# Performance work log

Measured on AMD Instinct MI355X. Metric: run time of the kernel, lower is better.

## Reference

```python
import jax, jax.numpy as jnp
import numpy as np

N_LAYERS = 3


def setup_inputs() -> dict:
    key = jax.random.key(0)
    ks = jax.random.split(key, 7)
    n_users, n_items, d = 200000, 100000, 64
    n_nodes = n_users + n_items
    n_edges = 2000000
    return {
        "user_embeddings_weight": jax.random.normal(ks[0], (n_users, d), dtype=jnp.float32) * 0.1,
        "item_embeddings_weight": jax.random.normal(ks[1], (n_items, d), dtype=jnp.float32) * 0.1,
        "adj_vals": jax.random.uniform(ks[2], (n_edges,), dtype=jnp.float32),
        "adj_rows": jax.random.randint(ks[3], (n_edges,), 0, n_nodes, dtype=jnp.int32),
        "adj_cols": jax.random.randint(ks[4], (n_edges,), 0, n_nodes, dtype=jnp.int32),
        "user_indices": jax.random.randint(ks[5], (16384,), 0, n_users, dtype=jnp.int32),
        "item_indices": jax.random.randint(ks[6], (16384,), 0, n_items, dtype=jnp.int32),
    }


def reference(user_embeddings_weight, item_embeddings_weight, adj_vals, adj_rows, adj_cols, user_indices, item_indices):
    n_users = user_embeddings_weight.shape[0]
    n_nodes = n_users + item_embeddings_weight.shape[0]
    # layer-0 embeddings: concat users then items -> (N, d)
    emb = jnp.concatenate([user_embeddings_weight, item_embeddings_weight], axis=0)
    acc = emb  # running sum over layers (fuses stack+mean)
    cur = emb
    for _ in range(N_LAYERS):
        # SpMM in COO form: out[r] += val * cur[c]
        cur = jax.ops.segment_sum(adj_vals[:, None] * cur[adj_cols], adj_rows, num_segments=n_nodes)
        acc = acc + cur
    final = acc / jnp.float32(N_LAYERS + 1)  # mean over (n_layers+1) layer outputs
    user_emb = final[:n_users][user_indices]
    item_emb = final[n_users:][item_indices]
    return (user_emb, item_emb)
```

## Files before the change

### kernel.cpp

```cpp
#include <hip/hip_runtime.h>

#define D 64
#define RB 512
#define RB_SHIFT 9
#define COL_BITS 19
#define COL_MASK ((1u << COL_BITS) - 1u)
#define CAP 4096
#define NBMAX 640
#define TILE 4096

__device__ __forceinline__ float bf_lo(unsigned u) { return __uint_as_float(u << 16); }
__device__ __forceinline__ float bf_hi(unsigned u) { return __uint_as_float(u & 0xffff0000u); }
__device__ __forceinline__ unsigned pack_bf2(float a, float b) {
    unsigned ua = __float_as_uint(a), ub = __float_as_uint(b);
    ua += 0x7fffu + ((ua >> 16) & 1u);
    ub += 0x7fffu + ((ub >> 16) & 1u);
    return (ua >> 16) | (ub & 0xffff0000u);
}


__global__ __launch_bounds__(256) void k_tobf(
    const float* __restrict__ src, unsigned* __restrict__ dst, int n2)
{
    int stride = gridDim.x * 256;
    for (int i = blockIdx.x * 256 + threadIdx.x; i < n2; i += stride) {
        float2 v = ((const float2*)src)[i];
        dst[i] = pack_bf2(v.x, v.y);
    }
}

__global__ __launch_bounds__(256) void k_gather_init(
    const float* __restrict__ uw, const float* __restrict__ iw,
    const int* __restrict__ ui, const int* __restrict__ ii,
    float* __restrict__ out, int nq)
{
    int t = blockIdx.x * 256 + threadIdx.x;
    int total = nq * D;
    if (t < total) {
        int q = t >> 6, d = t & 63;
        out[t] = uw[ui[q] * D + d];
    } else if (t < 2 * total) {
        int u = t - total;
        int q = u >> 6, d = u & 63;
        out[t] = iw[ii[q] * D + d];
    }
}

__global__ __launch_bounds__(256) void k_gather_acc_bf(
    const uint2* __restrict__ src,
    const int* __restrict__ ui, const int* __restrict__ ii,
    int n_users, float* __restrict__ out, int nq, float scale)
{
    int lane16 = threadIdx.x & 15;
    int q = blockIdx.x * 16 + (threadIdx.x >> 4);
    if (q >= 2 * nq) return;
    int node = (q < nq) ? ui[q] : n_users + ii[q - nq];
    uint2 x = src[(size_t)node * 16 + lane16];
    float4* o = (float4*)&out[(size_t)q * D + lane16 * 4];
    float4 v = *o;
    v.x = (v.x + bf_lo(x.x)) * scale;
    v.y = (v.y + bf_hi(x.x)) * scale;
    v.z = (v.z + bf_lo(x.y)) * scale;
    v.w = (v.w + bf_hi(x.y)) * scale;
    *o = v;
}


__global__ __launch_bounds__(256) void k_bcount(
    const int* __restrict__ rows, int* __restrict__ bcnt, int ne, int nb)
{
    __shared__ int sh[NBMAX];
    int tid = threadIdx.x;
    int base = blockIdx.x * TILE;
    int end = base + TILE; if (end > ne) end = ne;
    for (int b = tid; b < nb; b += 256) sh[b] = 0;
    __syncthreads();
    for (int e = base + tid; e < end; e += 256)
        atomicAdd(&sh[rows[e] >> RB_SHIFT], 1);
    __syncthreads();
    for (int b = tid; b < nb; b += 256)
        if (sh[b]) atomicAdd(&bcnt[b], sh[b]);
}

__global__ __launch_bounds__(1024) void k_bscan(
    const int* __restrict__ bcnt, int* __restrict__ bstart,
    int* __restrict__ bktFill, int nb)
{
    __shared__ int s[1024];
    int t = threadIdx.x;
    int v = (t < nb) ? bcnt[t] : 0;
    s[t] = v; __syncthreads();
    for (int off = 1; off < 1024; off <<= 1) {
        int x = (t >= off) ? s[t - off] : 0;
        __syncthreads();
        s[t] += x;
        __syncthreads();
    }
    int excl = s[t] - v;
    if (t <= nb) {
        bstart[t] = excl;
        if (t < nb) bktFill[t] = excl;
    }
}

__global__ __launch_bounds__(256) void k_binpart(
    const float* __restrict__ vals, const int* __restrict__ rows,
    const int* __restrict__ cols,
    int* __restrict__ bucketFill, int2* __restrict__ staging,
    int ne, int nb)
{
    __shared__ int shist[NBMAX];
    __shared__ int sgb[NBMAX];
    int tid = threadIdx.x;
    int base = blockIdx.x * TILE;

    for (int b = tid; b < nb; b += 256) shist[b] = 0;
    __syncthreads();

    int myb[TILE / 256];
    int myr[TILE / 256];
    for (int k = 0; k < TILE / 256; ++k) {
        int e = base + k * 256 + tid;
        int b = -1, r = 0;
        if (e < ne) {
            r = rows[e];
            b = r >> RB_SHIFT;
            atomicAdd(&shist[b], 1);
        }
        myb[k] = b; myr[k] = r;
    }
    __syncthreads();
    for (int b = tid; b < nb; b += 256) {
        int c = shist[b];
        sgb[b] = (c > 0) ? atomicAdd(&bucketFill[b], c) : 0;
        shist[b] = 0;
    }
    __syncthreads();
    for (int k = 0; k < TILE / 256; ++k) {
        int e = base + k * 256 + tid;
        if (e >= ne) continue;
        int b = myb[k];
        int lofs = atomicAdd(&shist[b], 1);
        int2 pk;
        pk.x = (int)((((unsigned)myr[k] & (RB - 1)) << COL_BITS) | (unsigned)cols[e]);
        pk.y = __float_as_int(vals[e]);
        staging[sgb[b] + lofs] = pk;
    }
}

__global__ __launch_bounds__(256) void k_place3(
    const int* __restrict__ bstart, const int2* __restrict__ staging,
    int* __restrict__ rstart, int* __restrict__ cnt,
    int2* __restrict__ cedge, int n_nodes, int ne)
{
    __shared__ int hist[RB];
    __shared__ int excl[RB];
    __shared__ int ss[256];
    __shared__ int2 ebuf[CAP];
    int tid = threadIdx.x;
    int b = blockIdx.x;
    int rowbase = b << RB_SHIFT;
    int s = bstart[b], e = bstart[b + 1];
    int m = e - s;

    for (int i = tid; i < RB; i += 256) hist[i] = 0;
    __syncthreads();
    for (int p = s + tid; p < e; p += 256)
        atomicAdd(&hist[((unsigned)staging[p].x) >> COL_BITS], 1);
    __syncthreads();

    int c0 = hist[2 * tid], c1 = hist[2 * tid + 1];
    int sum = c0 + c1;
    ss[tid] = sum; __syncthreads();
    for (int off = 1; off < 256; off <<= 1) {
        int x = (tid >= off) ? ss[tid - off] : 0;
        __syncthreads();
        ss[tid] += x;
        __syncthreads();
    }
    int ex = ss[tid] - sum;
    excl[2 * tid] = ex;
    excl[2 * tid + 1] = ex + c0;
    __syncthreads();

    for (int i = tid; i < RB; i += 256) {
        int r = rowbase + i;
        if (r < n_nodes) { rstart[r] = s + excl[i]; cnt[r] = hist[i]; }
    }
    __syncthreads();
    for (int i = tid; i < RB; i += 256) hist[i] = excl[i];
    __syncthreads();

    if (m <= CAP) {
        for (int p = s + tid; p < e; p += 256) {
            int2 pk = staging[p];
            int lr = ((unsigned)pk.x) >> COL_BITS;
            int pos = atomicAdd(&hist[lr], 1);
            pk.x = (int)((unsigned)pk.x & COL_MASK);
            ebuf[pos] = pk;
        }
        __syncthreads();
        for (int p = tid; p < m; p += 256)
            cedge[s + p] = ebuf[p];
    } else {
        for (int p = s + tid; p < e; p += 256) {
            int2 pk = staging[p];
            int lr = ((unsigned)pk.x) >> COL_BITS;
            int pos = atomicAdd(&hist[lr], 1);
            pk.x = (int)((unsigned)pk.x & COL_MASK);
            cedge[s + pos] = pk;
        }
    }
}

__global__ __launch_bounds__(256) void k_mark(
    const int* __restrict__ rstart, const int* __restrict__ cnt,
    const int2* __restrict__ cedge,
    const int* __restrict__ ui, const int* __restrict__ ii,
    int n_users, unsigned char* __restrict__ flag, int nq)
{
    int q = blockIdx.x * 256 + threadIdx.x;
    if (q >= 2 * nq) return;
    int node = (q < nq) ? ui[q] : n_users + ii[q - nq];
    flag[node] = 1;
    int s = rstart[node], dg = cnt[node];
    for (int j = 0; j < dg; ++j) flag[cedge[s + j].x] = 1;
}

__global__ __launch_bounds__(256) void k_spmm_bf(
    const int* __restrict__ rstart, const int* __restrict__ cnt,
    const int2* __restrict__ cedge,
    const uint2* __restrict__ src,
    uint2* __restrict__ dst, int n_nodes,
    const unsigned char* __restrict__ flag)
{
    int lane16 = threadIdx.x & 15;
    int row = blockIdx.x * 16 + (threadIdx.x >> 4);
    if (row >= n_nodes) return;
    if (flag && !flag[row]) return;

    int s = rstart[row], dg = cnt[row];
    float a0 = 0, a1 = 0, a2 = 0, a3 = 0;
    int j = 0;
    for (; j + 3 < dg; j += 4) {
        int2 e0 = cedge[s + j],     e1 = cedge[s + j + 1];
        int2 e2 = cedge[s + j + 2], e3 = cedge[s + j + 3];
        uint2 x0 = src[(size_t)e0.x * 16 + lane16];
        uint2 x1 = src[(size_t)e1.x * 16 + lane16];
        uint2 x2 = src[(size_t)e2.x * 16 + lane16];
        uint2 x3 = src[(size_t)e3.x * 16 + lane16];
        float v0 = __int_as_float(e0.y), v1 = __int_as_float(e1.y);
        float v2 = __int_as_float(e2.y), v3 = __int_as_float(e3.y);
        a0 += v0 * bf_lo(x0.x); a1 += v0 * bf_hi(x0.x); a2 += v0 * bf_lo(x0.y); a3 += v0 * bf_hi(x0.y);
        a0 += v1 * bf_lo(x1.x); a1 += v1 * bf_hi(x1.x); a2 += v1 * bf_lo(x1.y); a3 += v1 * bf_hi(x1.y);
        a0 += v2 * bf_lo(x2.x); a1 += v2 * bf_hi(x2.x); a2 += v2 * bf_lo(x2.y); a3 += v2 * bf_hi(x2.y);
        a0 += v3 * bf_lo(x3.x); a1 += v3 * bf_hi(x3.x); a2 += v3 * bf_lo(x3.y); a3 += v3 * bf_hi(x3.y);
    }
    for (; j < dg; ++j) {
        int2 e0 = cedge[s + j];
        uint2 x0 = src[(size_t)e0.x * 16 + lane16];
        float v0 = __int_as_float(e0.y);
        a0 += v0 * bf_lo(x0.x); a1 += v0 * bf_hi(x0.x); a2 += v0 * bf_lo(x0.y); a3 += v0 * bf_hi(x0.y);
    }
    uint2 o;
    o.x = pack_bf2(a0, a1);
    o.y = pack_bf2(a2, a3);
    dst[(size_t)row * 16 + lane16] = o;
}

__global__ __launch_bounds__(256) void k_final_bf(
    const int* __restrict__ rstart, const int* __restrict__ cnt,
    const int2* __restrict__ cedge,
    const uint2* __restrict__ src,
    const int* __restrict__ ui, const int* __restrict__ ii,
    int n_users, float* __restrict__ out, int nq, float scale)
{
    int lane16 = threadIdx.x & 15;
    int q = blockIdx.x * 16 + (threadIdx.x >> 4);
    if (q >= 2 * nq) return;
    int node = (q < nq) ? ui[q] : n_users + ii[q - nq];

    int s = rstart[node], dg = cnt[node];
    float4* op = (float4*)&out[(size_t)q * D + lane16 * 4];
    float4 a = *op;
    int j = 0;
    for (; j + 1 < dg; j += 2) {
        int2 e0 = cedge[s + j], e1 = cedge[s + j + 1];
        uint2 x0 = src[(size_t)e0.x * 16 + lane16];
        uint2 x1 = src[(size_t)e1.x * 16 + lane16];
        float v0 = __int_as_float(e0.y), v1 = __int_as_float(e1.y);
        a.x += v0 * bf_lo(x0.x) + v1 * bf_lo(x1.x);
        a.y += v0 * bf_hi(x0.x) + v1 * bf_hi(x1.x);
        a.z += v0 * bf_lo(x0.y) + v1 * bf_lo(x1.y);
        a.w += v0 * bf_hi(x0.y) + v1 * bf_hi(x1.y);
    }
    if (j < dg) {
        int2 e0 = cedge[s + j];
        uint2 x0 = src[(size_t)e0.x * 16 + lane16];
        float v0 = __int_as_float(e0.y);
        a.x += v0 * bf_lo(x0.x); a.y += v0 * bf_hi(x0.x);
        a.z += v0 * bf_lo(x0.y); a.w += v0 * bf_hi(x0.y);
    }
    a.x *= scale; a.y *= scale; a.z *= scale; a.w *= scale;
    *op = a;
}


__global__ __launch_bounds__(256) void k_gather_acc(
    const float* __restrict__ src,
    const int* __restrict__ ui, const int* __restrict__ ii,
    int n_users, float* __restrict__ out, int nq, float scale)
{
    int t = blockIdx.x * 256 + threadIdx.x;
    int total = nq * D;
    if (t < total) {
        int q = t >> 6, d = t & 63;
        out[t] = (out[t] + src[ui[q] * D + d]) * scale;
    } else if (t < 2 * total) {
        int u = t - total;
        int q = u >> 6, d = u & 63;
        out[t] = (out[t] + src[(n_users + ii[q]) * D + d]) * scale;
    }
}

__global__ __launch_bounds__(256) void k_spmm_l0(
    const float* __restrict__ vals, const int* __restrict__ rows,
    const int* __restrict__ cols,
    const float* __restrict__ uw, const float* __restrict__ iw, int n_users,
    float* __restrict__ dst, int n_edges)
{
    int total = n_edges * D;
    int stride = gridDim.x * 256;
    for (int t = blockIdx.x * 256 + threadIdx.x; t < total; t += stride) {
        int e = t >> 6, d = t & 63;
        float v = vals[e];
        int c = cols[e], r = rows[e];
        float x = (c < n_users) ? uw[c * D + d] : iw[(c - n_users) * D + d];
        atomicAdd(dst + r * D + d, v * x);
    }
}

__global__ __launch_bounds__(256) void k_spmm(
    const float* __restrict__ vals, const int* __restrict__ rows,
    const int* __restrict__ cols,
    const float* __restrict__ src, float* __restrict__ dst, int n_edges)
{
    int total = n_edges * D;
    int stride = gridDim.x * 256;
    for (int t = blockIdx.x * 256 + threadIdx.x; t < total; t += stride) {
        int e = t >> 6, d = t & 63;
        float v = vals[e];
        int c = cols[e], r = rows[e];
        atomicAdd(dst + r * D + d, v * src[c * D + d]);
    }
}


extern "C" void kernel_launch(void* const* d_in, const int* in_sizes, int n_in,
                              void* d_out, int out_size, void* d_ws, size_t ws_size,
                              hipStream_t stream) {
    const float* uw   = (const float*)d_in[0];
    const float* iw   = (const float*)d_in[1];
    const float* vals = (const float*)d_in[2];
    const int*   rows = (const int*)d_in[3];
    const int*   cols = (const int*)d_in[4];
    const int*   ui   = (const int*)d_in[5];
    const int*   ii   = (const int*)d_in[6];
    float* out = (float*)d_out;

    const int n_users = in_sizes[0] / D;
    const int n_items = in_sizes[1] / D;
    const int n_nodes = n_users + n_items;
    const int n_edges = in_sizes[2];
    const int nq      = in_sizes[5];

    const int nb = (n_nodes + RB - 1) / RB;

    size_t off = 0;
    int* cnt     = (int*)((char*)d_ws + off); off += (size_t)n_nodes * 4;
    int* rstart  = (int*)((char*)d_ws + off); off += (size_t)n_nodes * 4;
    int* bstart  = (int*)((char*)d_ws + off); off += 4096 * 4;
    int* bcnt    = (int*)((char*)d_ws + off); off += 4096 * 4;
    int* bktFill = (int*)((char*)d_ws + off); off += 4096 * 4;
    unsigned char* flag = (unsigned char*)((char*)d_ws + off);
    off += ((size_t)n_nodes + 255) & ~(size_t)255;
    size_t big = off;

    size_t coff = big;
    unsigned* embB  = (unsigned*)((char*)d_ws + coff); coff += (size_t)n_nodes * D * 2;
    unsigned* bufAh = (unsigned*)((char*)d_ws + coff); coff += (size_t)n_nodes * D * 2;
    unsigned* bufBh = (unsigned*)((char*)d_ws + coff); coff += (size_t)n_nodes * D * 2;
    int2* cedge   = (int2*)((char*)d_ws + coff); coff += (size_t)n_edges * 8;
    int2* staging = (int2*)((char*)d_ws + coff); coff += (size_t)n_edges * 8;

    size_t foff = big;
    float* bufA = (float*)((char*)d_ws + foff); foff += (size_t)n_nodes * D * 4;
    float* bufB = (float*)((char*)d_ws + foff); foff += (size_t)n_nodes * D * 4;

    const int gq = (2 * nq * D + 255) / 256;
    const bool csr_ok = (coff <= ws_size) && (nb < 1024) &&
                        (nb + 1 <= NBMAX) && (n_nodes < (1 << COL_BITS));

    if (csr_ok) {
        k_tobf<<<2048, 256, 0, stream>>>(uw, embB, n_users * (D / 2));
        k_tobf<<<2048, 256, 0, stream>>>(iw, embB + (size_t)n_users * (D / 2),
                                         n_items * (D / 2));

        hipMemsetAsync(bcnt, 0, 4096 * 4, stream);
        hipMemsetAsync(flag, 0, (size_t)n_nodes, stream);
        k_bcount<<<(n_edges + TILE - 1) / TILE, 256, 0, stream>>>(rows, bcnt, n_edges, nb);
        k_bscan<<<1, 1024, 0, stream>>>(bcnt, bstart, bktFill, nb);
        k_binpart<<<(n_edges + TILE - 1) / TILE, 256, 0, stream>>>(
            vals, rows, cols, bktFill, staging, n_edges, nb);
        k_place3<<<nb, 256, 0, stream>>>(bstart, staging, rstart, cnt,
                                         cedge, n_nodes, n_edges);
        k_mark<<<(2 * nq + 255) / 256, 256, 0, stream>>>(
            rstart, cnt, cedge, ui, ii, n_users, flag, nq);

        k_gather_init<<<gq, 256, 0, stream>>>(uw, iw, ui, ii, out, nq);

        const int gs = (n_nodes + 15) / 16;
        const int gq16 = (2 * nq + 15) / 16;
        k_spmm_bf<<<gs, 256, 0, stream>>>(rstart, cnt, cedge, (const uint2*)embB,
                                          (uint2*)bufAh, n_nodes, nullptr);
        k_gather_acc_bf<<<gq16, 256, 0, stream>>>((const uint2*)bufAh, ui, ii,
                                                  n_users, out, nq, 1.0f);
        k_spmm_bf<<<gs, 256, 0, stream>>>(rstart, cnt, cedge, (const uint2*)bufAh,
                                          (uint2*)bufBh, n_nodes, flag);
        k_gather_acc_bf<<<gq16, 256, 0, stream>>>((const uint2*)bufBh, ui, ii,
                                                  n_users, out, nq, 1.0f);
        k_final_bf<<<gq16, 256, 0, stream>>>(rstart, cnt, cedge, (const uint2*)bufBh,
                                             ui, ii, n_users, out, nq, 0.25f);
    } else {
        hipMemsetAsync(bufA, 0, 2 * (size_t)n_nodes * D * 4, stream);
        const int gs = 8192;
        k_gather_init<<<gq, 256, 0, stream>>>(uw, iw, ui, ii, out, nq);
        k_spmm_l0<<<gs, 256, 0, stream>>>(vals, rows, cols, uw, iw, n_users, bufA, n_edges);
        k_gather_acc<<<gq, 256, 0, stream>>>(bufA, ui, ii, n_users, out, nq, 1.0f);
        k_spmm<<<gs, 256, 0, stream>>>(vals, rows, cols, bufA, bufB, n_edges);
        k_gather_acc<<<gq, 256, 0, stream>>>(bufB, ui, ii, n_users, out, nq, 1.0f);
        hipMemsetAsync(bufA, 0, (size_t)n_nodes * D * 4, stream);
        k_spmm<<<gs, 256, 0, stream>>>(vals, rows, cols, bufB, bufA, n_edges);
        k_gather_acc<<<gq, 256, 0, stream>>>(bufA, ui, ii, n_users, out, nq, 0.25f);
    }
}
```

Baseline: 354.6 us.

## Fuse gather/accumulate into final kernel, widen SpMM loads to 16 bytes

```diff
diff --git a/kernel.cpp b/kernel.cpp
--- a/kernel.cpp
+++ b/kernel.cpp
@@ -19,50 +19,17 @@
 }
 
 
-__global__ __launch_bounds__(256) void k_tobf(
-    const float* __restrict__ src, unsigned* __restrict__ dst, int n2)
+__global__ __launch_bounds__(256) void k_tobf2(
+    const float* __restrict__ uw, const float* __restrict__ iw,
+    unsigned* __restrict__ dst, int n2u, int n2i)
 {
     int stride = gridDim.x * 256;
-    for (int i = blockIdx.x * 256 + threadIdx.x; i < n2; i += stride) {
-        float2 v = ((const float2*)src)[i];
+    int total = n2u + n2i;
+    for (int i = blockIdx.x * 256 + threadIdx.x; i < total; i += stride) {
+        float2 v = (i < n2u) ? ((const float2*)uw)[i]
+                             : ((const float2*)iw)[i - n2u];
         dst[i] = pack_bf2(v.x, v.y);
     }
-}
-
-__global__ __launch_bounds__(256) void k_gather_init(
-    const float* __restrict__ uw, const float* __restrict__ iw,
-    const int* __restrict__ ui, const int* __restrict__ ii,
-    float* __restrict__ out, int nq)
-{
-    int t = blockIdx.x * 256 + threadIdx.x;
-    int total = nq * D;
-    if (t < total) {
-        int q = t >> 6, d = t & 63;
-        out[t] = uw[ui[q] * D + d];
-    } else if (t < 2 * total) {
-        int u = t - total;
-        int q = u >> 6, d = u & 63;
-        out[t] = iw[ii[q] * D + d];
-    }
-}
-
-__global__ __launch_bounds__(256) void k_gather_acc_bf(
-    const uint2* __restrict__ src,
-    const int* __restrict__ ui, const int* __restrict__ ii,
-    int n_users, float* __restrict__ out, int nq, float scale)
-{
-    int lane16 = threadIdx.x & 15;
-    int q = blockIdx.x * 16 + (threadIdx.x >> 4);
-    if (q >= 2 * nq) return;
-    int node = (q < nq) ? ui[q] : n_users + ii[q - nq];
-    uint2 x = src[(size_t)node * 16 + lane16];
-    float4* o = (float4*)&out[(size_t)q * D + lane16 * 4];
-    float4 v = *o;
-    v.x = (v.x + bf_lo(x.x)) * scale;
-    v.y = (v.y + bf_hi(x.x)) * scale;
-    v.z = (v.z + bf_lo(x.y)) * scale;
-    v.w = (v.w + bf_hi(x.y)) * scale;
-    *o = v;
 }
 
 
@@ -227,84 +194,130 @@
     for (int j = 0; j < dg; ++j) flag[cedge[s + j].x] = 1;
 }
 
-__global__ __launch_bounds__(256) void k_spmm_bf(
+__global__ __launch_bounds__(256) void k_spmm_bf8(
     const int* __restrict__ rstart, const int* __restrict__ cnt,
     const int2* __restrict__ cedge,
-    const uint2* __restrict__ src,
-    uint2* __restrict__ dst, int n_nodes,
+    const uint4* __restrict__ src,
+    uint4* __restrict__ dst, int n_nodes,
     const unsigned char* __restrict__ flag)
 {
-    int lane16 = threadIdx.x & 15;
-    int row = blockIdx.x * 16 + (threadIdx.x >> 4);
+    int lane8 = threadIdx.x & 7;
+    int row = blockIdx.x * 32 + (threadIdx.x >> 3);
     if (row >= n_nodes) return;
     if (flag && !flag[row]) return;
 
     int s = rstart[row], dg = cnt[row];
-    float a0 = 0, a1 = 0, a2 = 0, a3 = 0;
+    float a0 = 0, a1 = 0, a2 = 0, a3 = 0, a4 = 0, a5 = 0, a6 = 0, a7 = 0;
     int j = 0;
     for (; j + 3 < dg; j += 4) {
         int2 e0 = cedge[s + j],     e1 = cedge[s + j + 1];
         int2 e2 = cedge[s + j + 2], e3 = cedge[s + j + 3];
-        uint2 x0 = src[(size_t)e0.x * 16 + lane16];
-        uint2 x1 = src[(size_t)e1.x * 16 + lane16];
-        uint2 x2 = src[(size_t)e2.x * 16 + lane16];
-        uint2 x3 = src[(size_t)e3.x * 16 + lane16];
+        uint4 x0 = src[(size_t)e0.x * 8 + lane8];
+        uint4 x1 = src[(size_t)e1.x * 8 + lane8];
+        uint4 x2 = src[(size_t)e2.x * 8 + lane8];
+        uint4 x3 = src[(size_t)e3.x * 8 + lane8];
         float v0 = __int_as_float(e0.y), v1 = __int_as_float(e1.y);
         float v2 = __int_as_float(e2.y), v3 = __int_as_float(e3.y);
         a0 += v0 * bf_lo(x0.x); a1 += v0 * bf_hi(x0.x); a2 += v0 * bf_lo(x0.y); a3 += v0 * bf_hi(x0.y);
+        a4 += v0 * bf_lo(x0.z); a5 += v0 * bf_hi(x0.z); a6 += v0 * bf_lo(x0.w); a7 += v0 * bf_hi(x0.w);
         a0 += v1 * bf_lo(x1.x); a1 += v1 * bf_hi(x1.x); a2 += v1 * bf_lo(x1.y); a3 += v1 * bf_hi(x1.y);
+        a4 += v1 * bf_lo(x1.z); a5 += v1 * bf_hi(x1.z); a6 += v1 * bf_lo(x1.w); a7 += v1 * bf_hi(x1.w);
         a0 += v2 * bf_lo(x2.x); a1 += v2 * bf_hi(x2.x); a2 += v2 * bf_lo(x2.y); a3 += v2 * bf_hi(x2.y);
+        a4 += v2 * bf_lo(x2.z); a5 += v2 * bf_hi(x2.z); a6 += v2 * bf_lo(x2.w); a7 += v2 * bf_hi(x2.w);
         a0 += v3 * bf_lo(x3.x); a1 += v3 * bf_hi(x3.x); a2 += v3 * bf_lo(x3.y); a3 += v3 * bf_hi(x3.y);
+        a4 += v3 * bf_lo(x3.z); a5 += v3 * bf_hi(x3.z); a6 += v3 * bf_lo(x3.w); a7 += v3 * bf_hi(x3.w);
     }
     for (; j < dg; ++j) {
         int2 e0 = cedge[s + j];
-        uint2 x0 = src[(size_t)e0.x * 16 + lane16];
+        uint4 x0 = src[(size_t)e0.x * 8 + lane8];
         float v0 = __int_as_float(e0.y);
         a0 += v0 * bf_lo(x0.x); a1 += v0 * bf_hi(x0.x); a2 += v0 * bf_lo(x0.y); a3 += v0 * bf_hi(x0.y);
-    }
-    uint2 o;
+        a4 += v0 * bf_lo(x0.z); a5 += v0 * bf_hi(x0.z); a6 += v0 * bf_lo(x0.w); a7 += v0 * bf_hi(x0.w);
+    }
+    uint4 o;
     o.x = pack_bf2(a0, a1);
     o.y = pack_bf2(a2, a3);
-    dst[(size_t)row * 16 + lane16] = o;
-}
-
-__global__ __launch_bounds__(256) void k_final_bf(
+    o.z = pack_bf2(a4, a5);
+    o.w = pack_bf2(a6, a7);
+    dst[(size_t)row * 8 + lane8] = o;
+}
+
+__global__ __launch_bounds__(256) void k_final_all(
     const int* __restrict__ rstart, const int* __restrict__ cnt,
     const int2* __restrict__ cedge,
-    const uint2* __restrict__ src,
+    const float* __restrict__ uw, const float* __restrict__ iw,
+    const uint4* __restrict__ bufA, const uint4* __restrict__ bufB,
     const int* __restrict__ ui, const int* __restrict__ ii,
     int n_users, float* __restrict__ out, int nq, float scale)
 {
-    int lane16 = threadIdx.x & 15;
-    int q = blockIdx.x * 16 + (threadIdx.x >> 4);
+    int lane8 = threadIdx.x & 7;
+    int q = blockIdx.x * 32 + (threadIdx.x >> 3);
     if (q >= 2 * nq) return;
     int node = (q < nq) ? ui[q] : n_users + ii[q - nq];
 
+    const float* embrow = (node < n_users) ? &uw[(size_t)node * D]
+                                           : &iw[(size_t)(node - n_users) * D];
+    float4 e0 = ((const float4*)embrow)[lane8 * 2];
+    float4 e1 = ((const float4*)embrow)[lane8 * 2 + 1];
+    uint4 xa = bufA[(size_t)node * 8 + lane8];
+    uint4 xb = bufB[(size_t)node * 8 + lane8];
+    float a0 = e0.x + bf_lo(xa.x) + bf_lo(xb.x);
+    float a1 = e0.y + bf_hi(xa.x) + bf_hi(xb.x);
+    float a2 = e0.z + bf_lo(xa.y) + bf_lo(xb.y);
+    float a3 = e0.w + bf_hi(xa.y) + bf_hi(xb.y);
+    float a4 = e1.x + bf_lo(xa.z) + bf_lo(xb.z);
+    float a5 = e1.y + bf_hi(xa.z) + bf_hi(xb.z);
+    float a6 = e1.z + bf_lo(xa.w) + bf_lo(xb.w);
+    float a7 = e1.w + bf_hi(xa.w) + bf_hi(xb.w);
+
     int s = rstart[node], dg = cnt[node];
-    float4* op = (float4*)&out[(size_t)q * D + lane16 * 4];
-    float4 a = *op;
     int j = 0;
     for (; j + 1 < dg; j += 2) {
-        int2 e0 = cedge[s + j], e1 = cedge[s + j + 1];
-        uint2 x0 = src[(size_t)e0.x * 16 + lane16];
-        uint2 x1 = src[(size_t)e1.x * 16 + lane16];
-        float v0 = __int_as_float(e0.y), v1 = __int_as_float(e1.y);
-        a.x += v0 * bf_lo(x0.x) + v1 * bf_lo(x1.x);
-        a.y += v0 * bf_hi(x0.x) + v1 * bf_hi(x1.x);
-        a.z += v0 * bf_lo(x0.y) + v1 * bf_lo(x1.y);
-        a.w += v0 * bf_hi(x0.y) + v1 * bf_hi(x1.y);
+        int2 ed0 = cedge[s + j], ed1 = cedge[s + j + 1];
+        uint4 x0 = bufB[(size_t)ed0.x * 8 + lane8];
+        uint4 x1 = bufB[(size_t)ed1.x * 8 + lane8];
+        float v0 = __int_as_float(ed0.y), v1 = __int_as_float(ed1.y);
+        a0 += v0 * bf_lo(x0.x) + v1 * bf_lo(x1.x);
+        a1 += v0 * bf_hi(x0.x) + v1 * bf_hi(x1.x);
+        a2 += v0 * bf_lo(x0.y) + v1 * bf_lo(x1.y);
+        a3 += v0 * bf_hi(x0.y) + v1 * bf_hi(x1.y);
+        a4 += v0 * bf_lo(x0.z) + v1 * bf_lo(x1.z);
+        a5 += v0 * bf_hi(x0.z) + v1 * bf_hi(x1.z);
+        a6 += v0 * bf_lo(x0.w) + v1 * bf_lo(x1.w);
+        a7 += v0 * bf_hi(x0.w) + v1 * bf_hi(x1.w);
     }
     if (j < dg) {
-        int2 e0 = cedge[s + j];
-        uint2 x0 = src[(size_t)e0.x * 16 + lane16];
-        float v0 = __int_as_float(e0.y);
-        a.x += v0 * bf_lo(x0.x); a.y += v0 * bf_hi(x0.x);
-        a.z += v0 * bf_lo(x0.y); a.w += v0 * bf_hi(x0.y);
-    }
-    a.x *= scale; a.y *= scale; a.z *= scale; a.w *= scale;
-    *op = a;
-}
-
+        int2 ed0 = cedge[s + j];
+        uint4 x0 = bufB[(size_t)ed0.x * 8 + lane8];
+        float v0 = __int_as_float(ed0.y);
+        a0 += v0 * bf_lo(x0.x); a1 += v0 * bf_hi(x0.x);
+        a2 += v0 * bf_lo(x0.y); a3 += v0 * bf_hi(x0.y);
+        a4 += v0 * bf_lo(x0.z); a5 += v0 * bf_hi(x0.z);
+        a6 += v0 * bf_lo(x0.w); a7 += v0 * bf_hi(x0.w);
+    }
+    float4 o0 = { a0 * scale, a1 * scale, a2 * scale, a3 * scale };
+    float4 o1 = { a4 * scale, a5 * scale, a6 * scale, a7 * scale };
+    ((float4*)&out[(size_t)q * D])[lane8 * 2] = o0;
+    ((float4*)&out[(size_t)q * D])[lane8 * 2 + 1] = o1;
+}
+
+
+__global__ __launch_bounds__(256) void k_gather_init(
+    const float* __restrict__ uw, const float* __restrict__ iw,
+    const int* __restrict__ ui, const int* __restrict__ ii,
+    float* __restrict__ out, int nq)
+{
+    int t = blockIdx.x * 256 + threadIdx.x;
+    int total = nq * D;
+    if (t < total) {
+        int q = t >> 6, d = t & 63;
+        out[t] = uw[ui[q] * D + d];
+    } else if (t < 2 * total) {
+        int u = t - total;
+        int q = u >> 6, d = u & 63;
+        out[t] = iw[ii[q] * D + d];
+    }
+}
 
 __global__ __launch_bounds__(256) void k_gather_acc(
     const float* __restrict__ src,
@@ -402,9 +415,8 @@
                         (nb + 1 <= NBMAX) && (n_nodes < (1 << COL_BITS));
 
     if (csr_ok) {
-        k_tobf<<<2048, 256, 0, stream>>>(uw, embB, n_users * (D / 2));
-        k_tobf<<<2048, 256, 0, stream>>>(iw, embB + (size_t)n_users * (D / 2),
-                                         n_items * (D / 2));
+        k_tobf2<<<2048, 256, 0, stream>>>(uw, iw, embB,
+                                          n_users * (D / 2), n_items * (D / 2));
 
         hipMemsetAsync(bcnt, 0, 4096 * 4, stream);
         hipMemsetAsync(flag, 0, (size_t)n_nodes, stream);
@@ -417,20 +429,15 @@
         k_mark<<<(2 * nq + 255) / 256, 256, 0, stream>>>(
             rstart, cnt, cedge, ui, ii, n_users, flag, nq);
 
-        k_gather_init<<<gq, 256, 0, stream>>>(uw, iw, ui, ii, out, nq);
-
-        const int gs = (n_nodes + 15) / 16;
-        const int gq16 = (2 * nq + 15) / 16;
-        k_spmm_bf<<<gs, 256, 0, stream>>>(rstart, cnt, cedge, (const uint2*)embB,
-                                          (uint2*)bufAh, n_nodes, nullptr);
-        k_gather_acc_bf<<<gq16, 256, 0, stream>>>((const uint2*)bufAh, ui, ii,
-                                                  n_users, out, nq, 1.0f);
-        k_spmm_bf<<<gs, 256, 0, stream>>>(rstart, cnt, cedge, (const uint2*)bufAh,
-                                          (uint2*)bufBh, n_nodes, flag);
-        k_gather_acc_bf<<<gq16, 256, 0, stream>>>((const uint2*)bufBh, ui, ii,
-                                                  n_users, out, nq, 1.0f);
-        k_final_bf<<<gq16, 256, 0, stream>>>(rstart, cnt, cedge, (const uint2*)bufBh,
-                                             ui, ii, n_users, out, nq, 0.25f);
+        const int gs32 = (n_nodes + 31) / 32;
+        const int gq32 = (2 * nq + 31) / 32;
+        k_spmm_bf8<<<gs32, 256, 0, stream>>>(rstart, cnt, cedge, (const uint4*)embB,
+                                             (uint4*)bufAh, n_nodes, nullptr);
+        k_spmm_bf8<<<gs32, 256, 0, stream>>>(rstart, cnt, cedge, (const uint4*)bufAh,
+                                             (uint4*)bufBh, n_nodes, flag);
+        k_final_all<<<gq32, 256, 0, stream>>>(rstart, cnt, cedge, uw, iw,
+                                              (const uint4*)bufAh, (const uint4*)bufBh,
+                                              ui, ii, n_users, out, nq, 0.25f);
     } else {
         hipMemsetAsync(bufA, 0, 2 * (size_t)n_nodes * D * 4, stream);
         const int gs = 8192;
```

Measured after the change: 320.9 us. -9.5%, faster.
